# Kernel tuning notes

Measured on AMD Instinct MI355X. Metric: run time of the kernel, lower is better.

Reference implementation:

```python
import jax, jax.numpy as jnp
import numpy as np

D, K = 512, 32


def setup_inputs() -> dict:
    key = jax.random.key(0)
    k1, k2, k3 = jax.random.split(key, 3)
    X = jax.random.normal(k1, (8, D, 128, 128), dtype=jnp.float32)
    std1 = 1.0 / (K * D) ** 0.5
    codewords = jax.random.uniform(k2, (K, D), dtype=jnp.float32, minval=-std1, maxval=std1)
    scale = jax.random.uniform(k3, (K,), dtype=jnp.float32, minval=-1.0, maxval=0.0)
    return {"X": X, "codewords": codewords, "scale": scale}


def reference(X, codewords, scale):
    B = X.shape[0]
    # [B, D, H, W] -> [B, N, D]
    Xf = X.reshape(B, D, -1).transpose(0, 2, 1)
    # scaled L2: s_k * ||x_i - d_k||^2, expanded to avoid [B,N,K,D] residuals
    x2 = jnp.sum(Xf * Xf, axis=-1, keepdims=True)            # [B, N, 1]
    c2 = jnp.sum(codewords * codewords, axis=-1)              # [K]
    xc = jnp.einsum('bnd,kd->bnk', Xf, codewords)             # [B, N, K]
    sl = scale * (x2 - 2.0 * xc + c2)                         # [B, N, K]
    A = jax.nn.softmax(sl, axis=2)                            # [B, N, K]
    # E[b,k,d] = sum_n A[b,n,k] * (X[b,n,d] - C[k,d])
    E = jnp.einsum('bnk,bnd->bkd', A, Xf) - jnp.sum(A, axis=1)[..., None] * codewords
    return E
```

## Files before the change

### kernel.cpp

```cpp
#include <hip/hip_runtime.h>
#include <stdint.h>

#define B_ 8
#define D_ 512
#define N_ 16384
#define K_ 32

typedef __attribute__((ext_vector_type(8))) short short8;
typedef __attribute__((ext_vector_type(16))) float f32x16;

union F8 { short8 v; unsigned short s[8]; uint32_t u[4]; uint4 q; };

__device__ __forceinline__ uint32_t bfpack2(float lo, float hi) {
    uint32_t a = __float_as_uint(lo);
    uint32_t b = __float_as_uint(hi);
    a += 0x7FFFu + ((a >> 16) & 1u);
    b += 0x7FFFu + ((b >> 16) & 1u);
    return (a >> 16) | (b & 0xFFFF0000u);
}

__launch_bounds__(256, 2)
__global__ void encode_kernel(const float* __restrict__ X,
                              const float* __restrict__ Cg,
                              const float* __restrict__ scale,
                              float* __restrict__ part,
                              float* __restrict__ aSumAcc)
{
    __shared__ uint32_t xsTw[D_ * 20];
    __shared__ float    lgp[4][32][36];
    __shared__ uint32_t A_ldsw[K_ * 20];
    __shared__ float    x2p[4][32];
    __shared__ float    scs[K_], c2s[K_];
    __shared__ float    c2tmp[K_][9];
    __shared__ float    aSumLds[K_];

    unsigned short* xsTs  = (unsigned short*)xsTw;
    unsigned short* A_lds = (unsigned short*)A_ldsw;

    const int tid = threadIdx.x;
    const int l   = tid & 63;
    const int w   = __builtin_amdgcn_readfirstlane(tid >> 6);
    const int lc  = l & 31;
    const int nh  = l >> 5;
    const int b     = blockIdx.x >> 6;
    const int chunk = blockIdx.x & 63;

    {
        int k = tid >> 3, dg = tid & 7;
        const float* cr = Cg + k * D_ + dg * 64;
        float s2 = 0.f;
#pragma unroll
        for (int i = 0; i < 16; ++i) {
            float4 v = *(const float4*)(cr + i * 4);
            s2 += v.x * v.x + v.y * v.y + v.z * v.z + v.w * v.w;
        }
        c2tmp[k][dg] = s2;
        if (tid < K_) { scs[tid] = scale[tid]; aSumLds[tid] = 0.f; }
    }
    __syncthreads();
    if (tid < K_) {
        float s = 0.f;
#pragma unroll
        for (int dg = 0; dg < 8; ++dg) s += c2tmp[tid][dg];
        c2s[tid] = s;
    }

    F8 cfr[8];
#pragma unroll
    for (int ss = 0; ss < 8; ++ss) {
        int d0 = (8 * w + ss) * 16 + nh * 8;
        const float* cp = Cg + lc * D_ + d0;
        float4 a  = *(const float4*)(cp);
        float4 bq = *(const float4*)(cp + 4);
        cfr[ss].u[0] = bfpack2(a.x, a.y);
        cfr[ss].u[1] = bfpack2(a.z, a.w);
        cfr[ss].u[2] = bfpack2(bq.x, bq.y);
        cfr[ss].u[3] = bfpack2(bq.z, bq.w);
    }

    f32x16 eacc[4];
#pragma unroll
    for (int ti = 0; ti < 4; ++ti)
#pragma unroll
        for (int r = 0; r < 16; ++r) eacc[ti][r] = 0.f;
    float aSumReg[4] = {0.f, 0.f, 0.f, 0.f};

    const int nl  = l >> 3;
    const int kq  = l & 7;
    const int smn = w * 8 + nl;
    const int k0  = kq * 4;

    const int o  = tid >> 3;
    const int nq = tid & 7;
    const size_t xbase = (size_t)b * D_ * N_ + (size_t)chunk * 256;

    for (int t = 0; t < 8; ++t) {
        __syncthreads();

        {
            const float* Xp = X + xbase + t * 32 + nq * 4;
            float4 x2a; x2a.x = x2a.y = x2a.z = x2a.w = 0.f;
#pragma unroll
            for (int r = 0; r < 16; ++r) {
                int d = o + 32 * r;
                float4 v = *(const float4*)(Xp + (size_t)d * N_);
                x2a.x += v.x * v.x; x2a.y += v.y * v.y;
                x2a.z += v.z * v.z; x2a.w += v.w * v.w;
                uint2 p;
                p.x = bfpack2(v.x, v.y);
                p.y = bfpack2(v.z, v.w);
                *(uint2*)&xsTw[d * 20 + nq * 2] = p;
            }
#pragma unroll
            for (int m = 8; m <= 32; m <<= 1) {
                x2a.x += __shfl_xor(x2a.x, m);
                x2a.y += __shfl_xor(x2a.y, m);
                x2a.z += __shfl_xor(x2a.z, m);
                x2a.w += __shfl_xor(x2a.w, m);
            }
            if (l < 8) *(float4*)&x2p[w][nq * 4] = x2a;
        }
        __syncthreads();

        f32x16 lacc;
#pragma unroll
        for (int r = 0; r < 16; ++r) lacc[r] = 0.f;
#pragma unroll
        for (int ss = 0; ss < 8; ++ss) {
            int d0 = (8 * w + ss) * 16 + nh * 8;
            F8 af;
#pragma unroll
            for (int j = 0; j < 8; ++j)
                af.s[j] = xsTs[(d0 + j) * 40 + lc];
            lacc = __builtin_amdgcn_mfma_f32_32x32x16_bf16(af.v, cfr[ss].v, lacc, 0, 0, 0);
        }
#pragma unroll
        for (int r = 0; r < 16; ++r)
            lgp[w][(r & 3) + 8 * (r >> 2) + 4 * nh][lc] = lacc[r];
        __syncthreads();

        {
            float4 xc = *(const float4*)&lgp[0][smn][k0];
            float4 x1 = *(const float4*)&lgp[1][smn][k0];
            float4 x2q = *(const float4*)&lgp[2][smn][k0];
            float4 x3 = *(const float4*)&lgp[3][smn][k0];
            xc.x += x1.x + x2q.x + x3.x;
            xc.y += x1.y + x2q.y + x3.y;
            xc.z += x1.z + x2q.z + x3.z;
            xc.w += x1.w + x2q.w + x3.w;
            float x2v = x2p[0][smn] + x2p[1][smn] + x2p[2][smn] + x2p[3][smn];
            float sl0 = scs[k0]     * (x2v - 2.f * xc.x + c2s[k0]);
            float sl1 = scs[k0 + 1] * (x2v - 2.f * xc.y + c2s[k0 + 1]);
            float sl2 = scs[k0 + 2] * (x2v - 2.f * xc.z + c2s[k0 + 2]);
            float sl3 = scs[k0 + 3] * (x2v - 2.f * xc.w + c2s[k0 + 3]);
            float m = fmaxf(fmaxf(sl0, sl1), fmaxf(sl2, sl3));
#pragma unroll
            for (int mk = 1; mk <= 4; mk <<= 1) m = fmaxf(m, __shfl_xor(m, mk));
            float e0 = __expf(sl0 - m), e1 = __expf(sl1 - m);
            float e2 = __expf(sl2 - m), e3 = __expf(sl3 - m);
            float s = e0 + e1 + e2 + e3;
#pragma unroll
            for (int mk = 1; mk <= 4; mk <<= 1) s += __shfl_xor(s, mk);
            float inv = 1.f / s;
            e0 *= inv; e1 *= inv; e2 *= inv; e3 *= inv;
            aSumReg[0] += e0; aSumReg[1] += e1;
            aSumReg[2] += e2; aSumReg[3] += e3;
            A_lds[(k0)     * 40 + smn] = (unsigned short)(bfpack2(e0, 0.f));
            A_lds[(k0 + 1) * 40 + smn] = (unsigned short)(bfpack2(e1, 0.f));
            A_lds[(k0 + 2) * 40 + smn] = (unsigned short)(bfpack2(e2, 0.f));
            A_lds[(k0 + 3) * 40 + smn] = (unsigned short)(bfpack2(e3, 0.f));
        }
        __syncthreads();

#pragma unroll
        for (int ti = 0; ti < 4; ++ti) {
            int dcol = (4 * w + ti) * 32 + lc;
#pragma unroll
            for (int ns = 0; ns < 2; ++ns) {
                F8 af, bf;
                af.q = *(const uint4*)&A_lds[lc * 40 + ns * 16 + nh * 8];
                bf.q = *(const uint4*)&xsTs[dcol * 40 + ns * 16 + nh * 8];
                eacc[ti] = __builtin_amdgcn_mfma_f32_32x32x16_bf16(af.v, bf.v, eacc[ti], 0, 0, 0);
            }
        }
    }

    float* pB = part + (size_t)blockIdx.x * (K_ * D_);
#pragma unroll
    for (int ti = 0; ti < 4; ++ti) {
        int d = (4 * w + ti) * 32 + lc;
#pragma unroll
        for (int r = 0; r < 16; ++r) {
            int k = (r & 3) + 8 * (r >> 2) + 4 * nh;
            pB[k * D_ + d] = eacc[ti][r];
        }
    }

#pragma unroll
    for (int i = 0; i < 4; ++i) {
#pragma unroll
        for (int m = 8; m <= 32; m <<= 1) aSumReg[i] += __shfl_xor(aSumReg[i], m);
    }
    if (l < 8) {
#pragma unroll
        for (int i = 0; i < 4; ++i) unsafeAtomicAdd(&aSumLds[k0 + i], aSumReg[i]);
    }
    __syncthreads();
    if (tid < K_) unsafeAtomicAdd(&aSumAcc[b * K_ + tid], aSumLds[tid]);
}

__global__ void finish_kernel(const float* __restrict__ part,
                              const float* __restrict__ aSumAcc,
                              const float* __restrict__ Cg,
                              float* __restrict__ out)
{
    int idx = blockIdx.x * 256 + threadIdx.x;
    int kd = idx & (K_ * D_ - 1);
    int b  = idx >> 14;
    int k  = kd >> 9;
    const float* p = part + (size_t)b * 64 * (K_ * D_) + kd;
    float s = 0.f;
#pragma unroll 8
    for (int c = 0; c < 64; ++c) s += p[(size_t)c * (K_ * D_)];
    out[idx] = s - aSumAcc[(b << 5) + k] * Cg[kd];
}

extern "C" void kernel_launch(void* const* d_in, const int* in_sizes, int n_in,
                              void* d_out, int out_size, void* d_ws, size_t ws_size,
                              hipStream_t stream)
{
    const float* X  = (const float*)d_in[0];
    const float* C  = (const float*)d_in[1];
    const float* sc = (const float*)d_in[2];
    float* out = (float*)d_out;

    float* part    = (float*)d_ws;
    float* aSumAcc = part + (size_t)512 * K_ * D_;

    hipMemsetAsync(aSumAcc, 0, B_ * K_ * sizeof(float), stream);
    encode_kernel<<<B_ * 64, 256, 0, stream>>>(X, C, sc, part, aSumAcc);
    finish_kernel<<<(B_ * K_ * D_) / 256, 256, 0, stream>>>(part, aSumAcc, C, out);
}
```

Baseline: 385.4 us.

## Prefetch next X tile into registers and use LDS-only barriers

X loads for the next 32-column tile are issued into 16 float4 registers right after the current tile is staged to LDS. The loads then overlap with the MFMA logits, softmax and accumulation phases. The __syncthreads calls become custom barriers that wait only on LDS counters (waitcnt lgkmcnt), so outstanding global loads do not stall each barrier. This adds 64 VGPRs of live state and risks occupancy loss or spills under launch_bounds(256,2), and the last iteration issues a redundant reload.

```diff
diff --git a/kernel.cpp b/kernel.cpp
--- a/kernel.cpp
+++ b/kernel.cpp
@@ -17,6 +17,13 @@
     a += 0x7FFFu + ((a >> 16) & 1u);
     b += 0x7FFFu + ((b >> 16) & 1u);
     return (a >> 16) | (b & 0xFFFF0000u);
+}
+
+__device__ __forceinline__ void bar_lds() {
+    __builtin_amdgcn_sched_barrier(0);
+    __builtin_amdgcn_s_waitcnt(0xC07F);
+    __builtin_amdgcn_s_barrier();
+    __builtin_amdgcn_sched_barrier(0);
 }
 
 __launch_bounds__(256, 2)
@@ -94,16 +101,23 @@
     const int nq = tid & 7;
     const size_t xbase = (size_t)b * D_ * N_ + (size_t)chunk * 256;
 
+    float4 pf[16];
+    {
+        const float* Xp = X + xbase + nq * 4;
+#pragma unroll
+        for (int r = 0; r < 16; ++r)
+            pf[r] = *(const float4*)(Xp + (size_t)(o + 32 * r) * N_);
+    }
+
     for (int t = 0; t < 8; ++t) {
-        __syncthreads();
+        bar_lds();
 
         {
-            const float* Xp = X + xbase + t * 32 + nq * 4;
             float4 x2a; x2a.x = x2a.y = x2a.z = x2a.w = 0.f;
 #pragma unroll
             for (int r = 0; r < 16; ++r) {
                 int d = o + 32 * r;
-                float4 v = *(const float4*)(Xp + (size_t)d * N_);
+                float4 v = pf[r];
                 x2a.x += v.x * v.x; x2a.y += v.y * v.y;
                 x2a.z += v.z * v.z; x2a.w += v.w * v.w;
                 uint2 p;
@@ -120,7 +134,16 @@
             }
             if (l < 8) *(float4*)&x2p[w][nq * 4] = x2a;
         }
-        __syncthreads();
+
+        {
+            int tn = (t < 7) ? t + 1 : 7;
+            const float* Xp = X + xbase + tn * 32 + nq * 4;
+#pragma unroll
+            for (int r = 0; r < 16; ++r)
+                pf[r] = *(const float4*)(Xp + (size_t)(o + 32 * r) * N_);
+        }
+
+        bar_lds();
 
         f32x16 lacc;
 #pragma unroll
@@ -137,7 +160,8 @@
 #pragma unroll
         for (int r = 0; r < 16; ++r)
             lgp[w][(r & 3) + 8 * (r >> 2) + 4 * nh][lc] = lacc[r];
-        __syncthreads();
+
+        bar_lds();
 
         {
             float4 xc = *(const float4*)&lgp[0][smn][k0];
@@ -170,7 +194,8 @@
             A_lds[(k0 + 2) * 40 + smn] = (unsigned short)(bfpack2(e2, 0.f));
             A_lds[(k0 + 3) * 40 + smn] = (unsigned short)(bfpack2(e3, 0.f));
         }
-        __syncthreads();
+
+        bar_lds();
 
 #pragma unroll
         for (int ti = 0; ti < 4; ++ti) {
```

Result: no change. 385.9 us (+0.1%).
